# Kernel tuning notes

Hardware: AMD Instinct MI355X
Metric: run time of the kernel (lower is better)

The kernel has to match this reference:

```python
import jax, jax.numpy as jnp
import numpy as np

B, L, DM, H = 2, 2048, 512, 8
D = DM // H
FACTOR = 5
NUM_K = int(FACTOR * np.ceil(np.log(L)))  # 40
NUM_Q = NUM_K  # q_len == k_len here
EPS = 1e-5


def setup_inputs() -> dict:
    key = jax.random.key(0)
    ks = jax.random.split(key, 12)
    s = DM ** -0.5
    return {
        "q": jax.random.normal(ks[0], (B, L, DM), jnp.float32),
        "k": jax.random.normal(ks[1], (B, L, DM), jnp.float32),
        "v": jax.random.normal(ks[2], (B, L, DM), jnp.float32),
        "Wq": jax.random.normal(ks[3], (DM, DM), jnp.float32) * s,
        "bq": jnp.zeros((DM,), jnp.float32),
        "Wk": jax.random.normal(ks[4], (DM, DM), jnp.float32) * s,
        "bk": jnp.zeros((DM,), jnp.float32),
        "Wv": jax.random.normal(ks[5], (DM, DM), jnp.float32) * s,
        "bv": jnp.zeros((DM,), jnp.float32),
        "gamma": jnp.ones((DM,), jnp.float32),
        "beta": jnp.zeros((DM,), jnp.float32),
        "random_index": jax.random.randint(ks[6], (L, NUM_K), 0, L, jnp.int32),
    }


def _heads(x):
    # [B, L, DM] -> [B, H, L, D]
    return x.reshape(B, L, H, D).transpose(0, 2, 1, 3)


def reference(q, k, v, Wq, bq, Wk, bk, Wv, bv, gamma, beta, random_index):
    qp = _heads(q @ Wq + bq)
    kp = _heads(k @ Wk + bk)
    vp = _heads(v @ Wv + bv)

    # ProbSparse: sample NUM_K keys per query position (shared over batch/head)
    k_samp = kp[:, :, random_index, :]                      # [B,H,L,NUM_K,D]
    pre = jnp.einsum('bhid,bhijd->bhij', qp, k_samp)        # [B,H,L,NUM_K]
    measure = pre.max(-1) - pre.sum(-1) / L                 # sparsity measure [B,H,L]
    _, q_idx = jax.lax.top_k(measure, NUM_Q)                # [B,H,NUM_Q]

    q_sel = jnp.take_along_axis(qp, q_idx[..., None], axis=2)   # [B,H,NUM_Q,D]
    attn = jnp.einsum('bhid,bhjd->bhij', q_sel, kp) * D ** -0.5 # [B,H,NUM_Q,L]
    attn = jax.nn.softmax(attn, axis=-1)                    # dropout = identity (eval)
    out_sel = jnp.einsum('bhij,bhjd->bhid', attn, vp)       # [B,H,NUM_Q,D]

    # use_mask=False path: context is the mean of v over keys
    v_mean = vp.mean(axis=2)                                # [B,H,D]
    context = jnp.broadcast_to(v_mean[:, :, None, :], (B, H, L, D))
    bi = jnp.arange(B)[:, None, None]
    hi = jnp.arange(H)[None, :, None]
    out = context.at[bi, hi, q_idx].set(out_sel)            # scatter selected rows

    out = out.transpose(0, 2, 1, 3).reshape(B, L, DM)
    y = out + q
    mu = y.mean(-1, keepdims=True)
    var = y.var(-1, keepdims=True)
    yn = (y - mu) / jnp.sqrt(var + EPS) * gamma + beta
    return (yn, attn)
```

## Files before the change

### kernel.cpp

```cpp
#include <hip/hip_runtime.h>
#include <math.h>

#define BB 2
#define LL 2048
#define DMM 512
#define HH 8
#define DD 64
#define NUMK 40
#define NUMQ 40
#define LNEPS 1e-5f
#define LSEG 128
#define NLS 16

typedef unsigned short ushort_t;
typedef __attribute__((ext_vector_type(8))) short bf16x8;
typedef __attribute__((ext_vector_type(4))) float f32x4;

__device__ inline ushort_t f2bf(float x) {
    union { float f; unsigned int u; } v; v.f = x;
    unsigned int r = v.u + 0x7fffu + ((v.u >> 16) & 1u);
    return (ushort_t)(r >> 16);
}
__device__ inline float bf2f(ushort_t h) {
    union { unsigned int u; float f; } v; v.u = ((unsigned int)h) << 16;
    return v.f;
}

__global__ __launch_bounds__(256) void convert_w_kernel(
    const float* __restrict__ Wq, const float* __restrict__ Wk, const float* __restrict__ Wv,
    ushort_t* __restrict__ Wht, ushort_t* __restrict__ Wlt) {
    __shared__ float tile[64][65];
    const int idx = blockIdx.x;
    const int z = idx >> 6, rem = idx & 63;
    const size_t plane = (size_t)DMM * DMM;
    const float* W = (z == 0) ? Wq : (z == 1) ? Wk : Wv;
    ushort_t* wht = Wht + plane * z;
    ushort_t* wlt = Wlt + plane * z;
    const int n0 = (rem & 7) * 64, k0 = (rem >> 3) * 64;
    const int t = threadIdx.x;
    const int d = t & 63, g = t >> 6;
    for (int rr = g; rr < 64; rr += 4)
        tile[rr][d] = W[(size_t)(k0 + rr) * DMM + n0 + d];
    __syncthreads();
    for (int cc = g; cc < 64; cc += 4) {
        float x = tile[d][cc];
        ushort_t hi = f2bf(x);
        ushort_t lo = f2bf(x - bf2f(hi));
        wht[(size_t)(n0 + cc) * DMM + k0 + d] = hi;
        wlt[(size_t)(n0 + cc) * DMM + k0 + d] = lo;
    }
}

__device__ inline void stage_oneB(const ushort_t* __restrict__ g, ushort_t* lbuf,
                                  int r0, int lane, int k0) {
    const int r = r0 + (lane >> 3);
    const int c = (lane & 7) ^ (r & 7);
    const ushort_t* gp = g + (size_t)r * DMM + k0 + c * 8;
    __builtin_amdgcn_global_load_lds(
        (const __attribute__((address_space(1))) unsigned int*)gp,
        (__attribute__((address_space(3))) unsigned int*)(lbuf + (size_t)r0 * 64),
        16, 0, 0);
}
__device__ inline bf16x8 frag_ld(const ushort_t* buf, int row, int c) {
    const int idx = row * 8 + (c ^ (row & 7));
    return *(const bf16x8*)(buf + idx * 8);
}

__global__ __launch_bounds__(256, 2) void proj_mfma_kernel(
    const float* __restrict__ Xq, const float* __restrict__ Xk, const float* __restrict__ Xv,
    const ushort_t* __restrict__ Wht, const ushort_t* __restrict__ Wlt,
    const float* __restrict__ bq, const float* __restrict__ bk, const float* __restrict__ bv,
    float* __restrict__ Oq, float* __restrict__ Ok, float* __restrict__ Ov) {
    const int orig = blockIdx.x;
    const int c = (orig & 7) * 48 + (orig >> 3);
    const int jb = c & 3, mb = (c >> 2) & 31, z = c >> 7;

    const size_t wplane = (size_t)DMM * DMM;
    const float* X32 = (z == 0) ? Xq : (z == 1) ? Xk : Xv;
    const ushort_t* bh_g = Wht + wplane * z;
    const ushort_t* bl_g = Wlt + wplane * z;
    const float* bias = (z == 0) ? bq : (z == 1) ? bk : bv;
    float* Out = (z == 0) ? Oq : (z == 1) ? Ok : Ov;

    __shared__ __align__(16) ushort_t bufAh[128 * 64];
    __shared__ __align__(16) ushort_t bufAl[128 * 64];
    __shared__ __align__(16) ushort_t bufBh[128 * 64];
    __shared__ __align__(16) ushort_t bufBl[128 * 64];

    const int t = threadIdx.x;
    const int lane = t & 63, w = t >> 6;
    const int wm = (w & 1) * 64, wn = (w >> 1) * 64;
    const int m0 = mb * 128, j0 = jb * 128;

    const float* A32 = X32 + (size_t)m0 * DMM;
    const ushort_t* B_h = bh_g + (size_t)j0 * DMM;
    const ushort_t* B_l = bl_g + (size_t)j0 * DMM;

    const int ag = t & 7;
    const int ar = t >> 3;

    float4 a0[4], a1[4];
    auto load_a = [&](int k0v) {
#pragma unroll
        for (int kk = 0; kk < 4; ++kk) {
            const float* src = A32 + (size_t)(ar + 32 * kk) * DMM + k0v + ag * 8;
            a0[kk] = *(const float4*)src;
            a1[kk] = *(const float4*)(src + 4);
        }
    };
    auto write_a = [&]() {
#pragma unroll
        for (int kk = 0; kk < 4; ++kk) {
            const int r = ar + 32 * kk;
            const float xs[8] = {a0[kk].x, a0[kk].y, a0[kk].z, a0[kk].w,
                                 a1[kk].x, a1[kk].y, a1[kk].z, a1[kk].w};
            unsigned int hp[4], lp[4];
#pragma unroll
            for (int j = 0; j < 4; ++j) {
                const ushort_t h0 = f2bf(xs[2 * j]),     h1 = f2bf(xs[2 * j + 1]);
                const ushort_t l0 = f2bf(xs[2 * j] - bf2f(h0));
                const ushort_t l1 = f2bf(xs[2 * j + 1] - bf2f(h1));
                hp[j] = (unsigned int)h0 | ((unsigned int)h1 << 16);
                lp[j] = (unsigned int)l0 | ((unsigned int)l1 << 16);
            }
            const int slot = r * 8 + (ag ^ (r & 7));
            *(uint4*)(bufAh + slot * 8) = make_uint4(hp[0], hp[1], hp[2], hp[3]);
            *(uint4*)(bufAl + slot * 8) = make_uint4(lp[0], lp[1], lp[2], lp[3]);
        }
    };
    auto stage_b = [&](int k0v) {
#pragma unroll
        for (int i = 0; i < 4; ++i) {
            const int r0 = (w * 4 + i) * 8;
            stage_oneB(B_h, bufBh, r0, lane, k0v);
            stage_oneB(B_l, bufBl, r0, lane, k0v);
        }
    };

    f32x4 acc[4][4];
#pragma unroll
    for (int i = 0; i < 4; ++i)
#pragma unroll
        for (int j = 0; j < 4; ++j) acc[i][j] = (f32x4){0.f, 0.f, 0.f, 0.f};

    load_a(0);
    write_a();
    stage_b(0);

    for (int ch = 0; ch < 8; ++ch) {
        __syncthreads();
        if (ch < 7) load_a((ch + 1) * 64);
#pragma unroll
        for (int ks = 0; ks < 2; ++ks) {
            const int cc = ks * 4 + (lane >> 4);
            bf16x8 fah[4], fal[4];
#pragma unroll
            for (int tm = 0; tm < 4; ++tm) {
                const int row = wm + tm * 16 + (lane & 15);
                fah[tm] = frag_ld(bufAh, row, cc);
                fal[tm] = frag_ld(bufAl, row, cc);
            }
#pragma unroll
            for (int tn = 0; tn < 4; ++tn) {
                const int rowb = wn + tn * 16 + (lane & 15);
                const bf16x8 fbh = frag_ld(bufBh, rowb, cc);
                const bf16x8 fbl = frag_ld(bufBl, rowb, cc);
#pragma unroll
                for (int tm = 0; tm < 4; ++tm) {
                    acc[tm][tn] = __builtin_amdgcn_mfma_f32_16x16x32_bf16(fah[tm], fbh, acc[tm][tn], 0, 0, 0);
                    acc[tm][tn] = __builtin_amdgcn_mfma_f32_16x16x32_bf16(fal[tm], fbh, acc[tm][tn], 0, 0, 0);
                    acc[tm][tn] = __builtin_amdgcn_mfma_f32_16x16x32_bf16(fah[tm], fbl, acc[tm][tn], 0, 0, 0);
                }
            }
        }
        __syncthreads();
        if (ch < 7) { write_a(); stage_b((ch + 1) * 64); }
    }

#pragma unroll
    for (int tn = 0; tn < 4; ++tn) {
        const int gn = j0 + wn + tn * 16 + (lane & 15);
        const float bvv = bias[gn];
        const int h = gn >> 6, d = gn & 63;
#pragma unroll
        for (int tm = 0; tm < 4; ++tm) {
#pragma unroll
            for (int reg = 0; reg < 4; ++reg) {
                const int gm = m0 + wm + tm * 16 + (lane >> 4) * 4 + reg;
                const int b = gm >> 11, l = gm & (LL - 1);
                Out[(((size_t)(b * HH + h)) * LL + l) * DD + d] = acc[tm][tn][reg] + bvv;
            }
        }
    }
}

__global__ __launch_bounds__(256) void measure_vmean_kernel(
    const float* __restrict__ qp2, const float* __restrict__ kp2,
    const float* __restrict__ vp2, const int* __restrict__ rnd,
    float* __restrict__ measure, float* __restrict__ partial) {
    __shared__ float pv[256];
    const int bx = blockIdx.x;
    const int t = threadIdx.x;
    if (bx < 2048) {
        const int c = (bx & 7) * 256 + (bx >> 3);
        const int lane = t & 63;
        const int wv = t >> 6;
        const int g = lane >> 4;
        const int dq = (lane & 15) * 4;
        const int bh = c >> 7;
        const int i = (c & 127) * 16 + wv * 4 + g;
        const float4 qv = *(const float4*)(qp2 + ((size_t)bh * LL + i) * DD + dq);
        const float* kbase = kp2 + (size_t)bh * LL * DD;
        const int* rp = rnd + i * NUMK;
        float mx = -INFINITY, sm = 0.f;
#pragma unroll 8
        for (int j = 0; j < NUMK; ++j) {
            const int row = rp[j];
            const float4 kv = *(const float4*)(kbase + (size_t)row * DD + dq);
            float p = kv.x * qv.x;
            p = fmaf(kv.y, qv.y, p); p = fmaf(kv.z, qv.z, p); p = fmaf(kv.w, qv.w, p);
            p += __shfl_xor(p, 1, 64);
            p += __shfl_xor(p, 2, 64);
            p += __shfl_xor(p, 4, 64);
            p += __shfl_xor(p, 8, 64);
            mx = fmaxf(mx, p);
            sm += p;
        }
        if ((lane & 15) == 0) measure[(size_t)bh * LL + i] = mx - sm * (1.0f / LL);
    } else {
        const int idx = bx - 2048;
        const int chunk = idx & 31;
        const int bh = idx >> 5;
        const int d = t & 63, g = t >> 6;
        const int l0 = chunk * 64;
        float acc = 0.f;
        for (int l = l0 + g; l < l0 + 64; l += 4)
            acc += vp2[((size_t)bh * LL + l) * DD + d];
        pv[t] = acc;
        __syncthreads();
        if (t < 64)
            partial[(size_t)idx * 64 + t] = pv[t] + pv[64 + t] + pv[128 + t] + pv[192 + t];
    }
}

__global__ __launch_bounds__(256) void topk_kernel(const float* __restrict__ measure,
                                                   const float* __restrict__ partial,
                                                   int* __restrict__ q_idx,
                                                   int* __restrict__ sel_pos,
                                                   float* __restrict__ v_mean) {
    __shared__ unsigned int keys[LL];
    __shared__ int hist[256];
    __shared__ unsigned int prefix_sh;
    __shared__ int need_sh;
    __shared__ unsigned int cval[256];
    __shared__ int cidx[256];
    __shared__ int cnt;
    const int t = threadIdx.x;
    const int lane = t & 63;
    const int bh = blockIdx.x;
    for (int i = t; i < LL; i += 256) {
        const float f = measure[(size_t)bh * LL + i];
        unsigned int u = __float_as_uint(f);
        keys[i] = (u & 0x80000000u) ? ~u : (u | 0x80000000u);
        sel_pos[(size_t)bh * LL + i] = -1;
    }
    if (t < 64) {
        float s = 0.f;
        for (int c = 0; c < 32; ++c)
            s += partial[((size_t)bh * 32 + c) * 64 + t];
        v_mean[bh * 64 + t] = s * (1.0f / LL);
    }
    if (t == 0) { prefix_sh = 0u; need_sh = NUMQ; cnt = 0; }
    __syncthreads();

    for (int round = 0; round < 4; ++round) {
        const int shift = 24 - round * 8;
        hist[t] = 0;
        __syncthreads();
        const unsigned int pref = prefix_sh;
        if (round == 0) {
            for (int i = t; i < LL; i += 256) {
                const int b = (int)(keys[i] >> 24);
                unsigned long long rem = ~0ull;
                while (rem) {
                    const int leader = __ffsll((long long)rem) - 1;
                    const int b0 = __shfl(b, leader, 64);
                    const unsigned long long same = __ballot(b == b0) & rem;
                    if (lane == leader) atomicAdd(&hist[b0], (int)__popcll(same));
                    rem &= ~same;
                }
            }
        } else {
            const unsigned int mask = 0xFFFFFFFFu << (shift + 8);
            for (int i = t; i < LL; i += 256) {
                const unsigned int key = keys[i];
                if ((key & mask) == pref)
                    atomicAdd(&hist[(key >> shift) & 0xFF], 1);
            }
        }
        __syncthreads();
        if (t < 64) {
            const int b0 = hist[4 * t + 0], b1 = hist[4 * t + 1];
            const int b2 = hist[4 * t + 2], b3 = hist[4 * t + 3];
            const int loc = b0 + b1 + b2 + b3;
            int suf = loc;
#pragma unroll
            for (int off = 1; off < 64; off <<= 1) {
                const int other = __shfl_down(suf, off, 64);
                if (lane + off < 64) suf += other;
            }
            const int need = need_sh;
            int s[5];
            s[0] = suf;
            s[1] = suf - b0;
            s[2] = suf - b0 - b1;
            s[3] = suf - b0 - b1 - b2;
            s[4] = suf - loc;
#pragma unroll
            for (int kk = 0; kk < 4; ++kk) {
                if (s[kk] >= need && s[kk + 1] < need) {
                    need_sh = need - s[kk + 1];
                    prefix_sh = pref | ((unsigned int)(4 * t + kk) << shift);
                }
            }
        }
        __syncthreads();
    }
    const unsigned int K40 = prefix_sh;

    for (int i = t; i < LL; i += 256) {
        if (keys[i] >= K40) {
            int p = atomicAdd(&cnt, 1);
            if (p < 256) { cval[p] = keys[i]; cidx[p] = i; }
        }
    }
    __syncthreads();
    int M = cnt; if (M > 256) M = 256;
    for (int i = t; i < M; i += 256) {
        const unsigned int ki = cval[i];
        const int ii = cidx[i];
        int r = 0;
        for (int j = 0; j < M; ++j) {
            const unsigned int kj = cval[j];
            r += (kj > ki || (kj == ki && cidx[j] < ii)) ? 1 : 0;
        }
        if (r < NUMQ) {
            q_idx[bh * NUMQ + r] = ii;
            sel_pos[(size_t)bh * LL + ii] = r;
        }
    }
}

__global__ __launch_bounds__(256) void attn_part_kernel(
    const float* __restrict__ qp2, const float* __restrict__ kp2,
    const float* __restrict__ vp2, const int* __restrict__ q_idx,
    float* __restrict__ attn_out, float* __restrict__ part_m,
    float* __restrict__ part_s, float* __restrict__ part_pv) {
    __shared__ __align__(16) float Qs[NUMQ][68];
    __shared__ __align__(16) float Ks[LSEG * 64];
    __shared__ __align__(16) float Vs[LSEG * 64];
    __shared__ __align__(16) float Ss[NUMQ][136];
    const int t = threadIdx.x;
    const int lane = t & 63, w = t >> 6;
    const int bh = blockIdx.x;
    const int ls = blockIdx.y;
    const int l0 = ls * LSEG;

    for (int idx = t; idx < NUMQ * 16; idx += 256) {
        const int r = idx >> 4, c4 = idx & 15;
        const int qi = q_idx[bh * NUMQ + r];
        float4 v = *(const float4*)(qp2 + ((size_t)bh * LL + qi) * DD + c4 * 4);
        Qs[r][c4 * 4 + 0] = v.x * 0.125f;
        Qs[r][c4 * 4 + 1] = v.y * 0.125f;
        Qs[r][c4 * 4 + 2] = v.z * 0.125f;
        Qs[r][c4 * 4 + 3] = v.w * 0.125f;
    }

    const float* kseg = kp2 + ((size_t)bh * LL + l0) * DD;
    const float* vseg = vp2 + ((size_t)bh * LL + l0) * DD;
#pragma unroll
    for (int i = 0; i < 8; ++i) {
        const int r0 = (w * 8 + i) * 4;
        const int r = r0 + (lane >> 4);
        const int cg = (lane & 15) ^ (r & 15);
        __builtin_amdgcn_global_load_lds(
            (const __attribute__((address_space(1))) unsigned int*)(kseg + (size_t)r * DD + cg * 4),
            (__attribute__((address_space(3))) unsigned int*)(Ks + r0 * 64), 16, 0, 0);
        __builtin_amdgcn_global_load_lds(
            (const __attribute__((address_space(1))) unsigned int*)(vseg + (size_t)r * DD + cg * 4),
            (__attribute__((address_space(3))) unsigned int*)(Vs + r0 * 64), 16, 0, 0);
    }
    __syncthreads();

    const int qt = t >> 5;
    const int jt = t & 31;
    float acc[5][4];
#pragma unroll
    for (int i = 0; i < 5; ++i)
#pragma unroll
        for (int jj = 0; jj < 4; ++jj) acc[i][jj] = 0.f;

    for (int c4 = 0; c4 < 16; ++c4) {
        float4 q4[5];
#pragma unroll
        for (int i = 0; i < 5; ++i)
            q4[i] = *(const float4*)&Qs[qt + 8 * i][c4 * 4];
#pragma unroll
        for (int jj = 0; jj < 4; ++jj) {
            const int r = jt + 32 * jj;
            const float4 k4 = *(const float4*)&Ks[r * 64 + ((c4 ^ (r & 15)) * 4)];
#pragma unroll
            for (int i = 0; i < 5; ++i) {
                acc[i][jj] = fmaf(q4[i].x, k4.x, acc[i][jj]);
                acc[i][jj] = fmaf(q4[i].y, k4.y, acc[i][jj]);
                acc[i][jj] = fmaf(q4[i].z, k4.z, acc[i][jj]);
                acc[i][jj] = fmaf(q4[i].w, k4.w, acc[i][jj]);
            }
        }
    }

#pragma unroll
    for (int i = 0; i < 5; ++i) {
        const int r = qt + 8 * i;
        float m = fmaxf(fmaxf(acc[i][0], acc[i][1]), fmaxf(acc[i][2], acc[i][3]));
        m = fmaxf(m, __shfl_xor(m, 16, 64));
        m = fmaxf(m, __shfl_xor(m, 8, 64));
        m = fmaxf(m, __shfl_xor(m, 4, 64));
        m = fmaxf(m, __shfl_xor(m, 2, 64));
        m = fmaxf(m, __shfl_xor(m, 1, 64));
        float p0 = __expf(acc[i][0] - m), p1 = __expf(acc[i][1] - m);
        float p2 = __expf(acc[i][2] - m), p3 = __expf(acc[i][3] - m);
        Ss[r][jt]      = p0;
        Ss[r][jt + 32] = p1;
        Ss[r][jt + 64] = p2;
        Ss[r][jt + 96] = p3;
        float s = p0 + p1 + p2 + p3;
        s += __shfl_xor(s, 16, 64);
        s += __shfl_xor(s, 8, 64);
        s += __shfl_xor(s, 4, 64);
        s += __shfl_xor(s, 2, 64);
        s += __shfl_xor(s, 1, 64);
        if (jt == 0) {
            const int row = bh * NUMQ + r;
            part_m[row * NLS + ls] = m;
            part_s[row * NLS + ls] = s;
        }
    }
    __syncthreads();

    for (int idx = t; idx < NUMQ * 32; idx += 256) {
        const int r = idx >> 5, c4 = idx & 31;
        const float4 v = *(const float4*)&Ss[r][c4 * 4];
        *(float4*)(attn_out + (size_t)(bh * NUMQ + r) * LL + l0 + c4 * 4) = v;
    }

    const int dt = t & 31;
    float o[5][2];
#pragma unroll
    for (int i = 0; i < 5; ++i) { o[i][0] = 0.f; o[i][1] = 0.f; }
#pragma unroll 2
    for (int j0_ = 0; j0_ < LSEG; j0_ += 4) {
        float4 p4[5];
#pragma unroll
        for (int i = 0; i < 5; ++i)
            p4[i] = *(const float4*)&Ss[qt + 8 * i][j0_];
#pragma unroll
        for (int jj = 0; jj < 4; ++jj) {
            const int j = j0_ + jj;
            const int pg = (dt >> 1) ^ (j & 15);
            const float* vr = &Vs[j * 64 + pg * 4 + (dt & 1) * 2];
            const float v0 = vr[0], v1 = vr[1];
#pragma unroll
            for (int i = 0; i < 5; ++i) {
                const float p = ((const float*)&p4[i])[jj];
                o[i][0] = fmaf(p, v0, o[i][0]);
                o[i][1] = fmaf(p, v1, o[i][1]);
            }
        }
    }
#pragma unroll
    for (int i = 0; i < 5; ++i) {
        const int row = bh * NUMQ + qt + 8 * i;
        float* pp = part_pv + ((size_t)row * NLS + ls) * DD + dt * 2;
        pp[0] = o[i][0];
        pp[1] = o[i][1];
    }
}

__global__ __launch_bounds__(512) void final_all_kernel(
    const float* __restrict__ q_in, const int* __restrict__ sel_pos,
    const float* __restrict__ part_m, const float* __restrict__ part_s,
    const float* __restrict__ part_pv, const float* __restrict__ v_mean,
    const float* __restrict__ gamma, const float* __restrict__ beta,
    float* __restrict__ attn_out, float* __restrict__ yout) {
    __shared__ float wred[8];
    const int bx = blockIdx.x;
    const int j = threadIdx.x;
    if (bx >= BB * LL) {
        const int row = bx - BB * LL;
        float M = -INFINITY;
#pragma unroll
        for (int i = 0; i < NLS; ++i) M = fmaxf(M, part_m[row * NLS + i]);
        float T = 0.f;
#pragma unroll
        for (int i = 0; i < NLS; ++i)
            T += part_s[row * NLS + i] * __expf(part_m[row * NLS + i] - M);
        const float inv = 1.0f / T;
        const int s0 = j >> 5;
        const float g = __expf(part_m[row * NLS + s0] - M) * inv;
        float* arow = attn_out + (size_t)row * LL;
        float4 v = *(const float4*)&arow[4 * j];
        v.x *= g; v.y *= g; v.z *= g; v.w *= g;
        *(float4*)&arow[4 * j] = v;
        return;
    }
    const int lane = j & 63, wv = j >> 6;
    const int tok = bx;
    const int b = tok >> 11;
    const int l = tok & (LL - 1);
    const int h = wv, d = lane;
    const int bh = b * HH + h;
    const int p = sel_pos[(size_t)bh * LL + l];
    float val;
    if (p >= 0) {
        const int row = bh * NUMQ + p;
        float M = -INFINITY;
#pragma unroll
        for (int i = 0; i < NLS; ++i) M = fmaxf(M, part_m[row * NLS + i]);
        float T = 0.f, s = 0.f;
#pragma unroll
        for (int i = 0; i < NLS; ++i) {
            const float e = __expf(part_m[row * NLS + i] - M);
            T += part_s[row * NLS + i] * e;
            s += part_pv[((size_t)row * NLS + i) * DD + d] * e;
        }
        val = s * (1.0f / T);
    } else {
        val = v_mean[bh * DD + d];
    }
    float y = val + q_in[(size_t)tok * DMM + j];
    float s = y;
#pragma unroll
    for (int off = 32; off > 0; off >>= 1) s += __shfl_xor(s, off, 64);
    if (lane == 0) wred[wv] = s;
    __syncthreads();
    float tot = 0.f;
#pragma unroll
    for (int u = 0; u < 8; ++u) tot += wred[u];
    float mu = tot * (1.0f / DMM);
    __syncthreads();
    float dv = y - mu;
    float s2 = dv * dv;
#pragma unroll
    for (int off = 32; off > 0; off >>= 1) s2 += __shfl_xor(s2, off, 64);
    if (lane == 0) wred[wv] = s2;
    __syncthreads();
    float tot2 = 0.f;
#pragma unroll
    for (int u = 0; u < 8; ++u) tot2 += wred[u];
    float var = tot2 * (1.0f / DMM);
    float yn = dv * rsqrtf(var + LNEPS) * gamma[j] + beta[j];
    yout[(size_t)tok * DMM + j] = yn;
}

extern "C" void kernel_launch(void* const* d_in, const int* in_sizes, int n_in,
                              void* d_out, int out_size, void* d_ws, size_t ws_size,
                              hipStream_t stream) {
    const float* q     = (const float*)d_in[0];
    const float* k     = (const float*)d_in[1];
    const float* v     = (const float*)d_in[2];
    const float* Wq    = (const float*)d_in[3];
    const float* bq    = (const float*)d_in[4];
    const float* Wk    = (const float*)d_in[5];
    const float* bk    = (const float*)d_in[6];
    const float* Wv    = (const float*)d_in[7];
    const float* bv    = (const float*)d_in[8];
    const float* gamma = (const float*)d_in[9];
    const float* beta  = (const float*)d_in[10];
    const int*   rnd   = (const int*)d_in[11];

    float* ws = (float*)d_ws;
    const size_t proj_sz = (size_t)BB * HH * LL * DD;
    float* qp2     = ws;
    float* kp2     = qp2 + proj_sz;
    float* vp2     = kp2 + proj_sz;
    float* measure = vp2 + proj_sz;
    float* out_sel = measure + (size_t)BB * HH * LL;
    float* v_mean  = out_sel + (size_t)BB * HH * NUMQ * DD;
    float* partial = v_mean + (size_t)BB * HH * DD;
    float* part_m  = partial + (size_t)BB * HH * 32 * 64;
    float* part_s  = part_m + (size_t)BB * HH * NUMQ * NLS;
    float* part_pv = part_s + (size_t)BB * HH * NUMQ * NLS;
    int*   q_idx   = (int*)(part_pv + (size_t)BB * HH * NUMQ * NLS * DD);
    int*   sel_pos = q_idx + BB * HH * NUMQ;
    ushort_t* Wht = (ushort_t*)(sel_pos + BB * HH * LL);
    ushort_t* Wlt = Wht + 3 * (size_t)DMM * DMM;

    float* yn_out   = (float*)d_out;
    float* attn_out = yn_out + (size_t)BB * LL * DMM;

    convert_w_kernel<<<192, 256, 0, stream>>>(Wq, Wk, Wv, Wht, Wlt);
    proj_mfma_kernel<<<dim3(3 * (BB * LL / 128) * (DMM / 128), 1, 1), 256, 0, stream>>>(
        q, k, v, Wht, Wlt, bq, bk, bv, qp2, kp2, vp2);
    measure_vmean_kernel<<<2048 + 512, 256, 0, stream>>>(qp2, kp2, vp2, rnd, measure, partial);
    topk_kernel<<<BB * HH, 256, 0, stream>>>(measure, partial, q_idx, sel_pos, v_mean);
    attn_part_kernel<<<dim3(BB * HH, NLS), 256, 0, stream>>>(
        qp2, kp2, vp2, q_idx, attn_out, part_m, part_s, part_pv);
    final_all_kernel<<<BB * LL + BB * HH * NUMQ, 512, 0, stream>>>(
        q, sel_pos, part_m, part_s, part_pv, v_mean, gamma, beta, attn_out, yn_out);
}
```

Before: 180.8 us.

## Stage fp32 A tiles directly to LDS and split bf16 at fragment load

In the projection GEMM, the register-prefetched A tile with its per-thread bf16 hi/lo split is replaced. A is now copied as fp32 straight into swizzled LDS with global_load_lds, and split into hi/lo bf16 fragments only when each fragment is read. This removes the register staging and the A-side LDS write code, but it drops the overlap of the next chunk's loads with current compute and repeats the conversion for every wave that reads the same A rows. The attention partial kernel gets an XCD-aware flattened block index and issues the V segment load after the K barrier, so V loads overlap the QK compute.

```diff
diff --git a/kernel.cpp b/kernel.cpp
--- a/kernel.cpp
+++ b/kernel.cpp
@@ -65,6 +65,20 @@
     const int idx = row * 8 + (c ^ (row & 7));
     return *(const bf16x8*)(buf + idx * 8);
 }
+__device__ inline void frag_ld_cvt(const float* buf, int row, int cc,
+                                   bf16x8& fh, bf16x8& fl) {
+    const int s0 = (2 * cc)     ^ (row & 15);
+    const int s1 = (2 * cc + 1) ^ (row & 15);
+    const float4 x0 = *(const float4*)(buf + row * 64 + s0 * 4);
+    const float4 x1 = *(const float4*)(buf + row * 64 + s1 * 4);
+    const float xs[8] = {x0.x, x0.y, x0.z, x0.w, x1.x, x1.y, x1.z, x1.w};
+#pragma unroll
+    for (int j = 0; j < 8; ++j) {
+        const ushort_t h = f2bf(xs[j]);
+        fh[j] = (short)h;
+        fl[j] = (short)f2bf(xs[j] - bf2f(h));
+    }
+}
 
 __global__ __launch_bounds__(256, 2) void proj_mfma_kernel(
     const float* __restrict__ Xq, const float* __restrict__ Xk, const float* __restrict__ Xv,
@@ -82,8 +96,7 @@
     const float* bias = (z == 0) ? bq : (z == 1) ? bk : bv;
     float* Out = (z == 0) ? Oq : (z == 1) ? Ok : Ov;
 
-    __shared__ __align__(16) ushort_t bufAh[128 * 64];
-    __shared__ __align__(16) ushort_t bufAl[128 * 64];
+    __shared__ __align__(16) float    bufA[128 * 64];
     __shared__ __align__(16) ushort_t bufBh[128 * 64];
     __shared__ __align__(16) ushort_t bufBl[128 * 64];
 
@@ -96,60 +109,32 @@
     const ushort_t* B_h = bh_g + (size_t)j0 * DMM;
     const ushort_t* B_l = bl_g + (size_t)j0 * DMM;
 
-    const int ag = t & 7;
-    const int ar = t >> 3;
-
-    float4 a0[4], a1[4];
-    auto load_a = [&](int k0v) {
-#pragma unroll
-        for (int kk = 0; kk < 4; ++kk) {
-            const float* src = A32 + (size_t)(ar + 32 * kk) * DMM + k0v + ag * 8;
-            a0[kk] = *(const float4*)src;
-            a1[kk] = *(const float4*)(src + 4);
-        }
-    };
-    auto write_a = [&]() {
-#pragma unroll
-        for (int kk = 0; kk < 4; ++kk) {
-            const int r = ar + 32 * kk;
-            const float xs[8] = {a0[kk].x, a0[kk].y, a0[kk].z, a0[kk].w,
-                                 a1[kk].x, a1[kk].y, a1[kk].z, a1[kk].w};
-            unsigned int hp[4], lp[4];
-#pragma unroll
-            for (int j = 0; j < 4; ++j) {
-                const ushort_t h0 = f2bf(xs[2 * j]),     h1 = f2bf(xs[2 * j + 1]);
-                const ushort_t l0 = f2bf(xs[2 * j] - bf2f(h0));
-                const ushort_t l1 = f2bf(xs[2 * j + 1] - bf2f(h1));
-                hp[j] = (unsigned int)h0 | ((unsigned int)h1 << 16);
-                lp[j] = (unsigned int)l0 | ((unsigned int)l1 << 16);
-            }
-            const int slot = r * 8 + (ag ^ (r & 7));
-            *(uint4*)(bufAh + slot * 8) = make_uint4(hp[0], hp[1], hp[2], hp[3]);
-            *(uint4*)(bufAl + slot * 8) = make_uint4(lp[0], lp[1], lp[2], lp[3]);
-        }
-    };
-    auto stage_b = [&](int k0v) {
+    f32x4 acc[4][4];
+#pragma unroll
+    for (int i = 0; i < 4; ++i)
+#pragma unroll
+        for (int j = 0; j < 4; ++j) acc[i][j] = (f32x4){0.f, 0.f, 0.f, 0.f};
+
+    for (int ch = 0; ch < 8; ++ch) {
+        const int k0 = ch * 64;
+#pragma unroll
+        for (int i = 0; i < 8; ++i) {
+            const int r0 = (w * 8 + i) * 4;
+            const int r = r0 + (lane >> 4);
+            const int cg = (lane & 15) ^ (r & 15);
+            const float* gp = A32 + (size_t)r * DMM + k0 + cg * 4;
+            __builtin_amdgcn_global_load_lds(
+                (const __attribute__((address_space(1))) unsigned int*)gp,
+                (__attribute__((address_space(3))) unsigned int*)(bufA + (size_t)r0 * 64),
+                16, 0, 0);
+        }
 #pragma unroll
         for (int i = 0; i < 4; ++i) {
             const int r0 = (w * 4 + i) * 8;
-            stage_oneB(B_h, bufBh, r0, lane, k0v);
-            stage_oneB(B_l, bufBl, r0, lane, k0v);
-        }
-    };
-
-    f32x4 acc[4][4];
-#pragma unroll
-    for (int i = 0; i < 4; ++i)
-#pragma unroll
-        for (int j = 0; j < 4; ++j) acc[i][j] = (f32x4){0.f, 0.f, 0.f, 0.f};
-
-    load_a(0);
-    write_a();
-    stage_b(0);
-
-    for (int ch = 0; ch < 8; ++ch) {
+            stage_oneB(B_h, bufBh, r0, lane, k0);
+            stage_oneB(B_l, bufBl, r0, lane, k0);
+        }
         __syncthreads();
-        if (ch < 7) load_a((ch + 1) * 64);
 #pragma unroll
         for (int ks = 0; ks < 2; ++ks) {
             const int cc = ks * 4 + (lane >> 4);
@@ -157,8 +142,7 @@
 #pragma unroll
             for (int tm = 0; tm < 4; ++tm) {
                 const int row = wm + tm * 16 + (lane & 15);
-                fah[tm] = frag_ld(bufAh, row, cc);
-                fal[tm] = frag_ld(bufAl, row, cc);
+                frag_ld_cvt(bufA, row, cc, fah[tm], fal[tm]);
             }
 #pragma unroll
             for (int tn = 0; tn < 4; ++tn) {
@@ -174,7 +158,6 @@
             }
         }
         __syncthreads();
-        if (ch < 7) { write_a(); stage_b((ch + 1) * 64); }
     }
 
 #pragma unroll
@@ -362,8 +345,10 @@
     __shared__ __align__(16) float Ss[NUMQ][136];
     const int t = threadIdx.x;
     const int lane = t & 63, w = t >> 6;
-    const int bh = blockIdx.x;
-    const int ls = blockIdx.y;
+    const int orig = blockIdx.x;
+    const int cc_ = (orig & 7) * 32 + (orig >> 3);
+    const int bh = cc_ >> 4;
+    const int ls = cc_ & 15;
     const int l0 = ls * LSEG;
 
     for (int idx = t; idx < NUMQ * 16; idx += 256) {
@@ -386,11 +371,18 @@
         __builtin_amdgcn_global_load_lds(
             (const __attribute__((address_space(1))) unsigned int*)(kseg + (size_t)r * DD + cg * 4),
             (__attribute__((address_space(3))) unsigned int*)(Ks + r0 * 64), 16, 0, 0);
+    }
+    __syncthreads();
+
+#pragma unroll
+    for (int i = 0; i < 8; ++i) {
+        const int r0 = (w * 8 + i) * 4;
+        const int r = r0 + (lane >> 4);
+        const int cg = (lane & 15) ^ (r & 15);
         __builtin_amdgcn_global_load_lds(
             (const __attribute__((address_space(1))) unsigned int*)(vseg + (size_t)r * DD + cg * 4),
             (__attribute__((address_space(3))) unsigned int*)(Vs + r0 * 64), 16, 0, 0);
     }
-    __syncthreads();
 
     const int qt = t >> 5;
     const int jt = t & 31;
@@ -604,7 +596,7 @@
         q, k, v, Wht, Wlt, bq, bk, bv, qp2, kp2, vp2);
     measure_vmean_kernel<<<2048 + 512, 256, 0, stream>>>(qp2, kp2, vp2, rnd, measure, partial);
     topk_kernel<<<BB * HH, 256, 0, stream>>>(measure, partial, q_idx, sel_pos, v_mean);
-    attn_part_kernel<<<dim3(BB * HH, NLS), 256, 0, stream>>>(
+    attn_part_kernel<<<BB * HH * NLS, 256, 0, stream>>>(
         qp2, kp2, vp2, q_idx, attn_out, part_m, part_s, part_pv);
     final_all_kernel<<<BB * LL + BB * HH * NUMQ, 512, 0, stream>>>(
         q, sel_pos, part_m, part_s, part_pv, v_mean, gamma, beta, attn_out, yn_out);
```

Measured after the change: 183.8 us. No clear change (+1.7%).
